# Optimization experiments

Hardware: AMD Instinct MI355X
Metric: run time of the kernel (lower is better)

## Reference

```python
import jax, jax.numpy as jnp
import numpy as np

N_PER_VIEW = 8192
N_VIEWS = 3
N = N_PER_VIEW * N_VIEWS  # 24576 homogeneous nodes
E = 393216
R = 6          # num_relations
B = 8          # num_bases
PROJ = 128     # proj_dim
HEADS = 4
OUT = 32
HO = HEADS * OUT  # 128
LABELS = 4
NEG_SLOPE = 0.2


def setup_inputs() -> dict:
    key = jax.random.key(0)
    ks = jax.random.split(key, 32)
    inp = {}
    inp["x0"] = jax.random.normal(ks[0], (N_PER_VIEW, 2000), jnp.float32)
    inp["x1"] = jax.random.normal(ks[1], (N_PER_VIEW, 1500), jnp.float32)
    inp["x2"] = jax.random.normal(ks[2], (N_PER_VIEW, 500), jnp.float32)
    inp["edge_index"] = jax.random.randint(ks[3], (2, E), 0, N, jnp.int32)
    inp["edge_type"] = jax.random.randint(ks[4], (E,), 0, R, jnp.int32)
    # per-view projection params (pyg.nn.Linear: y = x @ W.T + b)
    inp["Wp0"] = jax.random.normal(ks[5], (PROJ, 2000), jnp.float32) * 0.02
    inp["bp0"] = jnp.zeros((PROJ,), jnp.float32)
    inp["Wp1"] = jax.random.normal(ks[6], (PROJ, 1500), jnp.float32) * 0.02
    inp["bp1"] = jnp.zeros((PROJ,), jnp.float32)
    inp["Wp2"] = jax.random.normal(ks[7], (PROJ, 500), jnp.float32) * 0.02
    inp["bp2"] = jnp.zeros((PROJ,), jnp.float32)
    # RGATConv layer 0 (in = PROJ = 128)
    inp["basis0"] = jax.random.normal(ks[8], (B, PROJ, HO), jnp.float32) * 0.05
    inp["comp0"] = jax.random.normal(ks[9], (R, B), jnp.float32) * 0.3
    inp["q0"] = jax.random.normal(ks[10], (HO, HEADS), jnp.float32) * 0.1
    inp["k0"] = jax.random.normal(ks[11], (HO, HEADS), jnp.float32) * 0.1
    # RGATConv layer 1 (in = HO = 128)
    inp["basis1"] = jax.random.normal(ks[12], (B, HO, HO), jnp.float32) * 0.05
    inp["comp1"] = jax.random.normal(ks[13], (R, B), jnp.float32) * 0.3
    inp["q1"] = jax.random.normal(ks[14], (HO, HEADS), jnp.float32) * 0.1
    inp["k1"] = jax.random.normal(ks[15], (HO, HEADS), jnp.float32) * 0.1
    # LinearIntegration: concat views -> Linear(n_views*HO, n_classes)
    inp["Wc"] = jax.random.normal(ks[16], (LABELS, N_VIEWS * HO), jnp.float32) * 0.05
    inp["bc"] = jnp.zeros((LABELS,), jnp.float32)
    return inp


def _rgat_layer(x, src, dst, edge_type, basis, comp, q, k):
    """PyG RGATConv: basis-decomposed weights, additive self-attention,
    within-relation softmax, mod='f-scaled', heads concatenated."""
    w = jnp.einsum('rb,bio->rio', comp, basis)          # [R, in, H*O]
    xw = jnp.einsum('ni,rio->rno', x, w)                # [R, N, H*O]
    out_j = xw[edge_type, src]                          # [E, H*O] (source msg)
    out_i = xw[edge_type, dst]                          # [E, H*O] (target)
    alpha = jax.nn.leaky_relu(out_i @ q + out_j @ k, NEG_SLOPE)  # [E, H]
    # within-relation softmax over edges sharing (relation, dst)
    seg = edge_type.astype(jnp.int32) * N + dst
    nseg = R * N
    amax = jax.ops.segment_max(alpha, seg, num_segments=nseg)
    ex = jnp.exp(alpha - amax[seg])
    den = jax.ops.segment_sum(ex, seg, num_segments=nseg)
    a = ex / (den[seg] + 1e-16)
    # mod='f-scaled': scale by destination in-degree (over all relations)
    deg = jax.ops.segment_sum(jnp.ones((E,), x.dtype), dst, num_segments=N)
    a = a * deg[dst][:, None]
    msg = (a[:, :, None] * out_j.reshape(E, HEADS, OUT)).reshape(E, HO)
    return jax.ops.segment_sum(msg, dst, num_segments=N)  # [N, H*O]


def _forward(x0, x1, x2, Wp0, bp0, Wp1, bp1, Wp2, bp2,
             basis0, comp0, q0, k0, basis1, comp1, q1, k1, Wc, bc,
             src, dst, edge_type):
    h0 = jax.nn.relu(x0 @ Wp0.T + bp0)
    h1 = jax.nn.relu(x1 @ Wp1.T + bp1)
    h2 = jax.nn.relu(x2 @ Wp2.T + bp2)
    x = jnp.concatenate([h0, h1, h2], axis=0)           # [N, PROJ]
    x = _rgat_layer(x, src, dst, edge_type, basis0, comp0, q0, k0)
    x = _rgat_layer(x, src, dst, edge_type, basis1, comp1, q1, k1)
    views = x.reshape(N_VIEWS, N_PER_VIEW, HO)          # nodes grouped by view
    feat = jnp.transpose(views, (1, 0, 2)).reshape(N_PER_VIEW, N_VIEWS * HO)
    return feat @ Wc.T + bc                              # [N_per_view, LABELS]


def reference(x0, x1, x2, edge_index, edge_type, Wp0, bp0, Wp1, bp1, Wp2, bp2,
              basis0, comp0, q0, k0, basis1, comp1, q1, k1, Wc, bc):
    src, dst = edge_index[0], edge_index[1]
    return _forward(x0, x1, x2, Wp0, bp0, Wp1, bp1, Wp2, bp2,
                    basis0, comp0, q0, k0, basis1, comp1, q1, k1, Wc, bc,
                    src, dst, edge_type)
```

## Files before the change

kernel.cpp:

```cpp
#include <hip/hip_runtime.h>
#include <hip/hip_bf16.h>
#include <math.h>

#define N_NODES 24576
#define NPV 8192
#define E_EDGES 393216
#define R_REL 6
#define B_BASES 8
#define HEADS 4
#define NEG_SLOPE 0.2f
#define NX (N_NODES * 128)
#define NK (N_NODES * R_REL)
#define SCAN_BLOCKS (NK / 256)

typedef unsigned short ushort_t;
using short8 = __attribute__((ext_vector_type(8))) short;
using f32x4 = __attribute__((ext_vector_type(4))) float;

__device__ __forceinline__ float lrelu(float x) { return x >= 0.f ? x : NEG_SLOPE * x; }
__device__ __forceinline__ float b2f(ushort_t u) {
  unsigned int v = ((unsigned int)u) << 16;
  float f;
  __builtin_memcpy(&f, &v, 4);
  return f;
}
__device__ __forceinline__ ushort_t f2b(float f) {
  __hip_bfloat16 h = __float2bfloat16(f);
  ushort_t u;
  __builtin_memcpy(&u, &h, 2);
  return u;
}

__global__ __launch_bounds__(256) void gemm_proj_split(
    const float* __restrict__ x0, const float* __restrict__ x1,
    const float* __restrict__ x2, const float* __restrict__ w0,
    const float* __restrict__ w1, const float* __restrict__ w2,
    float* __restrict__ Ppart) {
  __shared__ __align__(16) ushort_t As[64 * 64];
  __shared__ __align__(16) ushort_t Ws[128 * 64];
  const int z = blockIdx.y;
  const float* A;
  const float* W;
  int K, kstart, ksteps;
  if (z < 4)      { A = x0; W = w0; K = 2000; kstart = z * 512;       ksteps = 8; }
  else if (z < 7) { A = x1; W = w1; K = 1500; kstart = (z - 4) * 512; ksteps = 8; }
  else            { A = x2; W = w2; K = 500;  kstart = (z - 7) * 256; ksteps = 4; }
  const int tid = threadIdx.x;
  const int wave = tid >> 6, lane = tid & 63;
  const int m0 = blockIdx.x * 64;

  f32x4 acc[8];
#pragma unroll
  for (int n = 0; n < 8; ++n) acc[n] = (f32x4){0.f, 0.f, 0.f, 0.f};

  for (int step = 0; step < ksteps; ++step) {
    const int k0 = kstart + (step << 6);
    __syncthreads();
#pragma unroll
    for (int q = 0; q < 2; ++q) {
      int s = q * 256 + tid;
      int row = s >> 3, ch = s & 7;
      int gk = k0 + ((ch ^ (row & 7)) << 3);
      const float* gp = A + (long)(m0 + row) * K + gk;
      short8 o;
      if (gk + 8 <= K) {
        float4 a = *reinterpret_cast<const float4*>(gp);
        float4 b = *reinterpret_cast<const float4*>(gp + 4);
        o[0] = (short)f2b(a.x); o[1] = (short)f2b(a.y);
        o[2] = (short)f2b(a.z); o[3] = (short)f2b(a.w);
        o[4] = (short)f2b(b.x); o[5] = (short)f2b(b.y);
        o[6] = (short)f2b(b.z); o[7] = (short)f2b(b.w);
      } else {
#pragma unroll
        for (int j = 0; j < 8; ++j)
          o[j] = (gk + j < K) ? (short)f2b(gp[j]) : (short)0;
      }
      *reinterpret_cast<short8*>(As + s * 8) = o;
    }
#pragma unroll
    for (int q = 0; q < 4; ++q) {
      int s = q * 256 + tid;
      int row = s >> 3, ch = s & 7;
      int gk = k0 + ((ch ^ (row & 7)) << 3);
      const float* gp = W + (long)row * K + gk;
      short8 o;
      if (gk + 8 <= K) {
        float4 a = *reinterpret_cast<const float4*>(gp);
        float4 b = *reinterpret_cast<const float4*>(gp + 4);
        o[0] = (short)f2b(a.x); o[1] = (short)f2b(a.y);
        o[2] = (short)f2b(a.z); o[3] = (short)f2b(a.w);
        o[4] = (short)f2b(b.x); o[5] = (short)f2b(b.y);
        o[6] = (short)f2b(b.z); o[7] = (short)f2b(b.w);
      } else {
#pragma unroll
        for (int j = 0; j < 8; ++j)
          o[j] = (gk + j < K) ? (short)f2b(gp[j]) : (short)0;
      }
      *reinterpret_cast<short8*>(Ws + s * 8) = o;
    }
    __syncthreads();
#pragma unroll
    for (int kk = 0; kk < 2; ++kk) {
      const int arow = wave * 16 + (lane & 15);
      const int ach = (kk * 4 + (lane >> 4)) ^ (arow & 7);
      short8 afrag = *reinterpret_cast<const short8*>(As + arow * 64 + ach * 8);
#pragma unroll
      for (int n = 0; n < 8; ++n) {
        const int brow = n * 16 + (lane & 15);
        const int bch = (kk * 4 + (lane >> 4)) ^ (brow & 7);
        short8 bfrag = *reinterpret_cast<const short8*>(Ws + brow * 64 + bch * 8);
        acc[n] = __builtin_amdgcn_mfma_f32_16x16x32_bf16(afrag, bfrag, acc[n], 0, 0, 0);
      }
    }
  }
  const int rbase = m0 + wave * 16 + (lane >> 4) * 4;
  const int cb = lane & 15;
  float* out = Ppart + (long)z * NPV * 128;
#pragma unroll
  for (int n = 0; n < 8; ++n) {
    int col = n * 16 + cb;
#pragma unroll
    for (int r = 0; r < 4; ++r)
      out[(long)(rbase + r) * 128 + col] = acc[n][r];
  }
}

__global__ __launch_bounds__(256) void proj_reduce(
    const float* __restrict__ Ppart, const float* __restrict__ b0,
    const float* __restrict__ b1, const float* __restrict__ b2,
    ushort_t* __restrict__ xb) {
  int t = blockIdx.x * blockDim.x + threadIdx.x;
  if (t >= N_NODES * 16) return;
  int n = t >> 4, c0 = (t & 15) * 8;
  int v = n >> 13, m = n & (NPV - 1);
  int zb, zc;
  const float* bias;
  if (v == 0) { zb = 0; zc = 4; bias = b0; }
  else if (v == 1) { zb = 4; zc = 3; bias = b1; }
  else { zb = 7; zc = 2; bias = b2; }
  float s[8];
#pragma unroll
  for (int j = 0; j < 8; ++j) s[j] = bias[c0 + j];
  for (int zz = 0; zz < zc; ++zz) {
    const float* p = Ppart + ((long)(zb + zz) * NPV + m) * 128 + c0;
    float4 a = *reinterpret_cast<const float4*>(p);
    float4 b = *reinterpret_cast<const float4*>(p + 4);
    s[0] += a.x; s[1] += a.y; s[2] += a.z; s[3] += a.w;
    s[4] += b.x; s[5] += b.y; s[6] += b.z; s[7] += b.w;
  }
  short8 o;
#pragma unroll
  for (int j = 0; j < 8; ++j) {
    float vv = s[j] > 0.f ? s[j] : 0.f;
    o[j] = (short)f2b(vv);
  }
  *reinterpret_cast<short8*>(xb + (long)n * 128 + c0) = o;
}

template <bool SPLIT, bool TABLES>
__global__ __launch_bounds__(256) void mfma_gemm_nt(
    const ushort_t* __restrict__ A, const ushort_t* __restrict__ W,
    float* __restrict__ Cacc, ushort_t* __restrict__ Cb,
    int Kp, int kChunk, long strideW, long strideCz,
    const float* __restrict__ qt, const float* __restrict__ kt,
    float* __restrict__ ai, float* __restrict__ aj) {
  __shared__ __align__(16) ushort_t As[64 * 64];
  __shared__ __align__(16) ushort_t Ws[128 * 64];
  const int tid = threadIdx.x;
  const int wave = tid >> 6, lane = tid & 63;
  const int m0 = blockIdx.x * 64;
  const int kbase = blockIdx.y * kChunk;
  const ushort_t* Wz = W + (long)blockIdx.z * strideW;

  f32x4 acc[8];
#pragma unroll
  for (int n = 0; n < 8; ++n) acc[n] = (f32x4){0.f, 0.f, 0.f, 0.f};

  for (int k0 = kbase; k0 < kbase + kChunk; k0 += 64) {
    __syncthreads();
#pragma unroll
    for (int q = 0; q < 2; ++q) {
      int s = q * 256 + tid;
      int row = s >> 3, ch = s & 7;
      int sch = ch ^ (row & 7);
      const ushort_t* g = A + (long)(m0 + row) * Kp + k0 + sch * 8;
      __builtin_amdgcn_global_load_lds(
          (const __attribute__((address_space(1))) unsigned int*)g,
          (__attribute__((address_space(3))) unsigned int*)(As + s * 8), 16, 0, 0);
    }
#pragma unroll
    for (int q = 0; q < 4; ++q) {
      int s = q * 256 + tid;
      int row = s >> 3, ch = s & 7;
      int sch = ch ^ (row & 7);
      const ushort_t* g = Wz + (long)row * Kp + k0 + sch * 8;
      __builtin_amdgcn_global_load_lds(
          (const __attribute__((address_space(1))) unsigned int*)g,
          (__attribute__((address_space(3))) unsigned int*)(Ws + s * 8), 16, 0, 0);
    }
    __syncthreads();
#pragma unroll
    for (int kk = 0; kk < 2; ++kk) {
      const int arow = wave * 16 + (lane & 15);
      const int ach = (kk * 4 + (lane >> 4)) ^ (arow & 7);
      short8 afrag = *reinterpret_cast<const short8*>(As + arow * 64 + ach * 8);
#pragma unroll
      for (int n = 0; n < 8; ++n) {
        const int brow = n * 16 + (lane & 15);
        const int bch = (kk * 4 + (lane >> 4)) ^ (brow & 7);
        short8 bfrag = *reinterpret_cast<const short8*>(Ws + brow * 64 + bch * 8);
        acc[n] = __builtin_amdgcn_mfma_f32_16x16x32_bf16(afrag, bfrag, acc[n], 0, 0, 0);
      }
    }
  }
  const int rbase = m0 + wave * 16 + (lane >> 4) * 4;
  const int cb = lane & 15;
  if (SPLIT) {
#pragma unroll
    for (int n = 0; n < 8; ++n) {
      int col = n * 16 + cb;
#pragma unroll
      for (int r = 0; r < 4; ++r)
        atomicAdd(&Cacc[(long)(rbase + r) * 128 + col], acc[n][r]);
    }
  } else {
    ushort_t* Cz = Cb + (long)blockIdx.z * strideCz;
#pragma unroll
    for (int n = 0; n < 8; ++n) {
      int col = n * 16 + cb;
#pragma unroll
      for (int r = 0; r < 4; ++r)
        Cz[(long)(rbase + r) * 128 + col] = f2b(acc[n][r]);
    }
  }
  if (TABLES) {
    float aq[4][4], ak[4][4];
#pragma unroll
    for (int r = 0; r < 4; ++r)
#pragma unroll
      for (int h = 0; h < 4; ++h) { aq[r][h] = 0.f; ak[r][h] = 0.f; }
#pragma unroll
    for (int n = 0; n < 8; ++n) {
      int col = n * 16 + cb;
      float4 qv = *reinterpret_cast<const float4*>(qt + (long)col * 4);
      float4 kv = *reinterpret_cast<const float4*>(kt + (long)col * 4);
#pragma unroll
      for (int r = 0; r < 4; ++r) {
        float x = acc[n][r];
        aq[r][0] += x * qv.x; aq[r][1] += x * qv.y;
        aq[r][2] += x * qv.z; aq[r][3] += x * qv.w;
        ak[r][0] += x * kv.x; ak[r][1] += x * kv.y;
        ak[r][2] += x * kv.z; ak[r][3] += x * kv.w;
      }
    }
#pragma unroll
    for (int mk = 1; mk < 16; mk <<= 1) {
#pragma unroll
      for (int r = 0; r < 4; ++r)
#pragma unroll
        for (int h = 0; h < 4; ++h) {
          aq[r][h] += __shfl_xor(aq[r][h], mk);
          ak[r][h] += __shfl_xor(ak[r][h], mk);
        }
    }
    int rr = cb >> 2, hh = cb & 3;
    long row = (long)blockIdx.z * N_NODES + rbase + rr;
    ai[row * 4 + hh] = aq[rr][hh];
    aj[row * 4 + hh] = ak[rr][hh];
  }
}

__global__ void fill_f32(float* __restrict__ p, long n, float v) {
  long i = blockIdx.x * (long)blockDim.x + threadIdx.x;
  long stride = (long)gridDim.x * blockDim.x;
  for (; i < n; i += stride) p[i] = v;
}

__global__ void compute_wT_b(const float* __restrict__ comp,
                             const float* __restrict__ basis,
                             ushort_t* __restrict__ wTb) {
  int idx = blockIdx.x * blockDim.x + threadIdx.x;
  if (idx >= R_REL * 128 * 128) return;
  int r = idx >> 14;
  int rem = idx & 16383;
  int o = rem >> 7;
  int i = rem & 127;
  float s = 0.f;
#pragma unroll
  for (int b = 0; b < B_BASES; ++b)
    s += comp[r * B_BASES + b] * basis[((b << 7) + i) * 128 + o];
  wTb[((long)(r << 7) + o) * 128 + i] = f2b(s);
}

__global__ void count_key(const int* __restrict__ dst, const int* __restrict__ et,
                          int* __restrict__ cnt, int E) {
  int e = blockIdx.x * blockDim.x + threadIdx.x;
  if (e < E) atomicAdd(&cnt[dst[e] * R_REL + et[e]], 1);
}

__global__ __launch_bounds__(256) void scan_block(const int* __restrict__ cnt,
                                                  int* __restrict__ start,
                                                  int* __restrict__ blockSums) {
  __shared__ int sm[256];
  const int t = threadIdx.x;
  const int i = blockIdx.x * 256 + t;
  int v = cnt[i];
  sm[t] = v;
  __syncthreads();
  for (int off = 1; off < 256; off <<= 1) {
    int u = (t >= off) ? sm[t - off] : 0;
    __syncthreads();
    sm[t] += u;
    __syncthreads();
  }
  start[i] = sm[t] - v;
  if (t == 255) blockSums[blockIdx.x] = sm[255];
}

__global__ __launch_bounds__(SCAN_BLOCKS) void scan_sums(int* __restrict__ blockSums) {
  __shared__ int sm[SCAN_BLOCKS];
  const int t = threadIdx.x;
  int v = blockSums[t];
  sm[t] = v;
  __syncthreads();
  for (int off = 1; off < SCAN_BLOCKS; off <<= 1) {
    int u = (t >= off) ? sm[t - off] : 0;
    __syncthreads();
    sm[t] += u;
    __syncthreads();
  }
  blockSums[t] = sm[t] - v;
}

__global__ __launch_bounds__(256) void add_offsets(int* __restrict__ start,
                                                   const int* __restrict__ blockSums) {
  int i = blockIdx.x * 256 + threadIdx.x;
  start[i] += blockSums[blockIdx.x];
  if (i == 0) start[NK] = E_EDGES;
}

__global__ void scatter_edges(const int* __restrict__ src, const int* __restrict__ dst,
                              const int* __restrict__ et, const int* __restrict__ start,
                              int* __restrict__ cursor, int* __restrict__ recs, int E) {
  int e = blockIdx.x * blockDim.x + threadIdx.x;
  if (e >= E) return;
  int key = dst[e] * R_REL + et[e];
  int pos = start[key] + atomicAdd(&cursor[key], 1);
  recs[pos] = src[e] | (et[e] << 16);
}

__global__ __launch_bounds__(256) void seg_softmax(
    const int* __restrict__ rstart, const int* __restrict__ recs,
    const float* __restrict__ ai, const float* __restrict__ aj,
    float* __restrict__ coef) {
  int seg = blockIdx.x * blockDim.x + threadIdx.x;
  if (seg >= NK) return;
  int p0 = rstart[seg], p1 = rstart[seg + 1];
  if (p0 == p1) return;
  int d = seg / R_REL, r = seg - d * R_REL;
  float4 av = *reinterpret_cast<const float4*>(ai + ((long)r * N_NODES + d) * 4);
  float degf = (float)(rstart[(d + 1) * R_REL] - rstart[d * R_REL]);
  float m[4] = {-INFINITY, -INFINITY, -INFINITY, -INFINITY};
  float sum[4] = {0.f, 0.f, 0.f, 0.f};
  for (int p = p0; p < p1; ++p) {
    int s = recs[p] & 0xFFFF;
    float4 bv = *reinterpret_cast<const float4*>(aj + ((long)r * N_NODES + s) * 4);
    float al[4] = {lrelu(av.x + bv.x), lrelu(av.y + bv.y),
                   lrelu(av.z + bv.z), lrelu(av.w + bv.w)};
#pragma unroll
    for (int h = 0; h < 4; ++h) {
      float nm = fmaxf(m[h], al[h]);
      sum[h] = sum[h] * __expf(m[h] - nm) + __expf(al[h] - nm);
      m[h] = nm;
    }
  }
  float rs[4];
#pragma unroll
  for (int h = 0; h < 4; ++h) rs[h] = degf / (sum[h] + 1e-16f);
  for (int p = p0; p < p1; ++p) {
    int s = recs[p] & 0xFFFF;
    float4 bv = *reinterpret_cast<const float4*>(aj + ((long)r * N_NODES + s) * 4);
    float al[4] = {lrelu(av.x + bv.x), lrelu(av.y + bv.y),
                   lrelu(av.z + bv.z), lrelu(av.w + bv.w)};
#pragma unroll
    for (int h = 0; h < 4; ++h)
      coef[(long)h * E_EDGES + p] = __expf(al[h] - m[h]) * rs[h];
  }
}

__global__ __launch_bounds__(256) void fused_agg(
    const int* __restrict__ rstart, const int* __restrict__ recs,
    const float* __restrict__ coef, const ushort_t* __restrict__ xwb,
    ushort_t* __restrict__ xb_out, float* __restrict__ fout) {
  const int wave = threadIdx.x >> 6, lane = threadIdx.x & 63;
  const int d = blockIdx.x * 4 + wave;
  const int s0 = rstart[d * R_REL], s1 = rstart[(d + 1) * R_REL];
  const float* cfp = coef + (long)(lane >> 4) * E_EDGES;
  float acc0 = 0.f, acc1 = 0.f;
#pragma unroll 4
  for (int pos = s0; pos < s1; ++pos) {
    int rec = recs[pos];
    float cf = cfp[pos];
    int s = rec & 0xFFFF, r = rec >> 16;
    unsigned int pk = *reinterpret_cast<const unsigned int*>(
        xwb + (((long)r * N_NODES + s) << 7) + 2 * lane);
    acc0 += cf * b2f((ushort_t)(pk & 0xFFFF));
    acc1 += cf * b2f((ushort_t)(pk >> 16));
  }
  if (xb_out) {
    unsigned int po = ((unsigned int)f2b(acc1) << 16) | (unsigned int)f2b(acc0);
    *reinterpret_cast<unsigned int*>(xb_out + ((long)d << 7) + 2 * lane) = po;
  }
  if (fout) {
    *reinterpret_cast<float2*>(fout + ((long)d << 7) + 2 * lane) =
        make_float2(acc0, acc1);
  }
}

__global__ void final_linear(const float* __restrict__ x, const float* __restrict__ Wc,
                             const float* __restrict__ bc, float* __restrict__ out) {
  __shared__ float wcs[4 * 384];
  for (int t = threadIdx.x; t < 4 * 384; t += blockDim.x) wcs[t] = Wc[t];
  __syncthreads();
  int i = blockIdx.x * blockDim.x + threadIdx.x;
  if (i >= NPV) return;
  float acc[4] = {0.f, 0.f, 0.f, 0.f};
  for (int v = 0; v < 3; ++v) {
    const float* xr = x + ((long)v * NPV + i) * 128;
    for (int c = 0; c < 128; c += 4) {
      float4 xv = *reinterpret_cast<const float4*>(xr + c);
#pragma unroll
      for (int l = 0; l < 4; ++l) {
        const float* w = wcs + l * 384 + v * 128 + c;
        acc[l] += xv.x * w[0] + xv.y * w[1] + xv.z * w[2] + xv.w * w[3];
      }
    }
  }
#pragma unroll
  for (int l = 0; l < 4; ++l) out[(long)i * 4 + l] = acc[l] + bc[l];
}

static void run_layer(const ushort_t* xb_in, ushort_t* xb_out, float* fout,
                      const float* basis, const float* comp, const float* q,
                      const float* k, ushort_t* xwb, ushort_t* wTb, float* ai,
                      float* aj, float* coef, const int* rstart, const int* recs,
                      hipStream_t stream) {
  compute_wT_b<<<(R_REL * 128 * 128 + 255) / 256, 256, 0, stream>>>(comp, basis, wTb);
  mfma_gemm_nt<false, true><<<dim3(N_NODES / 64, 1, R_REL), 256, 0, stream>>>(
      xb_in, wTb, nullptr, xwb, 128, 128, 128 * 128, (long)N_NODES * 128,
      q, k, ai, aj);
  seg_softmax<<<(NK + 255) / 256, 256, 0, stream>>>(rstart, recs, ai, aj, coef);
  fused_agg<<<N_NODES / 4, 256, 0, stream>>>(rstart, recs, coef, xwb, xb_out, fout);
}

extern "C" void kernel_launch(void* const* d_in, const int* in_sizes, int n_in,
                              void* d_out, int out_size, void* d_ws, size_t ws_size,
                              hipStream_t stream) {
  const float* x0 = (const float*)d_in[0];
  const float* x1 = (const float*)d_in[1];
  const float* x2 = (const float*)d_in[2];
  const int* edge_index = (const int*)d_in[3];
  const int* edge_type = (const int*)d_in[4];
  const float* Wp0 = (const float*)d_in[5];
  const float* bp0 = (const float*)d_in[6];
  const float* Wp1 = (const float*)d_in[7];
  const float* bp1 = (const float*)d_in[8];
  const float* Wp2 = (const float*)d_in[9];
  const float* bp2 = (const float*)d_in[10];
  const float* basis0 = (const float*)d_in[11];
  const float* comp0 = (const float*)d_in[12];
  const float* q0 = (const float*)d_in[13];
  const float* k0 = (const float*)d_in[14];
  const float* basis1 = (const float*)d_in[15];
  const float* comp1 = (const float*)d_in[16];
  const float* q1 = (const float*)d_in[17];
  const float* k1 = (const float*)d_in[18];
  const float* Wc = (const float*)d_in[19];
  const float* bc = (const float*)d_in[20];

  const int* src = edge_index;
  const int* dst = edge_index + E_EDGES;

  char* w = (char*)d_ws;
  auto alloc = [&](long bytes) {
    char* p = w;
    w += (bytes + 255) & ~255L;
    return p;
  };
  ushort_t* xbA  = (ushort_t*)alloc((long)NX * 2);
  ushort_t* xbB  = (ushort_t*)alloc((long)NX * 2);
  ushort_t* xwb  = (ushort_t*)alloc(9L * NPV * 128 * 4);
  ushort_t* wTb  = (ushort_t*)alloc((long)R_REL * 128 * 128 * 2);
  float* Cacc    = (float*)alloc((long)NX * 4);
  float* ai      = (float*)alloc((long)R_REL * N_NODES * 4 * 4);
  float* aj      = (float*)alloc((long)R_REL * N_NODES * 4 * 4);
  float* coef    = (float*)alloc((long)HEADS * E_EDGES * 4);
  int* cnt       = (int*)alloc((long)NK * 4);
  int* cursor    = (int*)alloc((long)NK * 4);
  int* rstart    = (int*)alloc((long)(NK + 1) * 4);
  int* recs      = (int*)alloc((long)E_EDGES * 4);
  int* blockSums = (int*)alloc((long)SCAN_BLOCKS * 4);
  float* Ppart   = (float*)xwb;

  gemm_proj_split<<<dim3(NPV / 64, 9), 256, 0, stream>>>(
      x0, x1, x2, Wp0, Wp1, Wp2, Ppart);
  proj_reduce<<<(N_NODES * 16 + 255) / 256, 256, 0, stream>>>(
      Ppart, bp0, bp1, bp2, xbA);

  fill_f32<<<96, 256, 0, stream>>>((float*)cnt, 2L * NK, 0.f);
  count_key<<<E_EDGES / 256, 256, 0, stream>>>(dst, edge_type, cnt, E_EDGES);
  scan_block<<<SCAN_BLOCKS, 256, 0, stream>>>(cnt, rstart, blockSums);
  scan_sums<<<1, SCAN_BLOCKS, 0, stream>>>(blockSums);
  add_offsets<<<SCAN_BLOCKS, 256, 0, stream>>>(rstart, blockSums);
  scatter_edges<<<E_EDGES / 256, 256, 0, stream>>>(src, dst, edge_type, rstart,
                                                   cursor, recs, E_EDGES);

  run_layer(xbA, xbB, nullptr, basis0, comp0, q0, k0, xwb, wTb, ai, aj, coef,
            rstart, recs, stream);
  run_layer(xbB, nullptr, Cacc, basis1, comp1, q1, k1, xwb, wTb, ai, aj, coef,
            rstart, recs, stream);

  final_linear<<<(NPV + 255) / 256, 256, 0, stream>>>(Cacc, Wc, bc, (float*)d_out);
}
```

Before: 278.5 us.

## Double-buffer LDS tiles and prefetch next K-slice into registers in projection GEMM

The split-K projection GEMM now loads the next K-slice from global memory into registers while MFMAs run on the current LDS buffer, then converts to bf16 and writes the other LDS buffer. This removes one barrier per step and hides global load latency behind compute. In exchange it doubles shared memory use and adds 48 float registers per thread, which may lower occupancy.

```diff
diff --git a/kernel.cpp b/kernel.cpp
--- a/kernel.cpp
+++ b/kernel.cpp
@@ -36,8 +36,8 @@
     const float* __restrict__ x2, const float* __restrict__ w0,
     const float* __restrict__ w1, const float* __restrict__ w2,
     float* __restrict__ Ppart) {
-  __shared__ __align__(16) ushort_t As[64 * 64];
-  __shared__ __align__(16) ushort_t Ws[128 * 64];
+  __shared__ __align__(16) ushort_t As[2][64 * 64];
+  __shared__ __align__(16) ushort_t Ws[2][128 * 64];
   const int z = blockIdx.y;
   const float* A;
   const float* W;
@@ -53,29 +53,26 @@
 #pragma unroll
   for (int n = 0; n < 8; ++n) acc[n] = (f32x4){0.f, 0.f, 0.f, 0.f};
 
-  for (int step = 0; step < ksteps; ++step) {
-    const int k0 = kstart + (step << 6);
-    __syncthreads();
+  float4 ra[4];
+  float4 rw[8];
+
+  auto LOADR = [&](int k0) {
 #pragma unroll
     for (int q = 0; q < 2; ++q) {
       int s = q * 256 + tid;
       int row = s >> 3, ch = s & 7;
       int gk = k0 + ((ch ^ (row & 7)) << 3);
       const float* gp = A + (long)(m0 + row) * K + gk;
-      short8 o;
       if (gk + 8 <= K) {
-        float4 a = *reinterpret_cast<const float4*>(gp);
-        float4 b = *reinterpret_cast<const float4*>(gp + 4);
-        o[0] = (short)f2b(a.x); o[1] = (short)f2b(a.y);
-        o[2] = (short)f2b(a.z); o[3] = (short)f2b(a.w);
-        o[4] = (short)f2b(b.x); o[5] = (short)f2b(b.y);
-        o[6] = (short)f2b(b.z); o[7] = (short)f2b(b.w);
+        ra[2 * q]     = *reinterpret_cast<const float4*>(gp);
+        ra[2 * q + 1] = *reinterpret_cast<const float4*>(gp + 4);
       } else {
-#pragma unroll
-        for (int j = 0; j < 8; ++j)
-          o[j] = (gk + j < K) ? (short)f2b(gp[j]) : (short)0;
+        float t[8];
+#pragma unroll
+        for (int j = 0; j < 8; ++j) t[j] = (gk + j < K) ? gp[j] : 0.f;
+        ra[2 * q]     = make_float4(t[0], t[1], t[2], t[3]);
+        ra[2 * q + 1] = make_float4(t[4], t[5], t[6], t[7]);
       }
-      *reinterpret_cast<short8*>(As + s * 8) = o;
     }
 #pragma unroll
     for (int q = 0; q < 4; ++q) {
@@ -83,36 +80,73 @@
       int row = s >> 3, ch = s & 7;
       int gk = k0 + ((ch ^ (row & 7)) << 3);
       const float* gp = W + (long)row * K + gk;
+      if (gk + 8 <= K) {
+        rw[2 * q]     = *reinterpret_cast<const float4*>(gp);
+        rw[2 * q + 1] = *reinterpret_cast<const float4*>(gp + 4);
+      } else {
+        float t[8];
+#pragma unroll
+        for (int j = 0; j < 8; ++j) t[j] = (gk + j < K) ? gp[j] : 0.f;
+        rw[2 * q]     = make_float4(t[0], t[1], t[2], t[3]);
+        rw[2 * q + 1] = make_float4(t[4], t[5], t[6], t[7]);
+      }
+    }
+  };
+
+  auto WRITELDS = [&](int buf) {
+#pragma unroll
+    for (int q = 0; q < 2; ++q) {
+      int s = q * 256 + tid;
       short8 o;
-      if (gk + 8 <= K) {
-        float4 a = *reinterpret_cast<const float4*>(gp);
-        float4 b = *reinterpret_cast<const float4*>(gp + 4);
-        o[0] = (short)f2b(a.x); o[1] = (short)f2b(a.y);
-        o[2] = (short)f2b(a.z); o[3] = (short)f2b(a.w);
-        o[4] = (short)f2b(b.x); o[5] = (short)f2b(b.y);
-        o[6] = (short)f2b(b.z); o[7] = (short)f2b(b.w);
-      } else {
-#pragma unroll
-        for (int j = 0; j < 8; ++j)
-          o[j] = (gk + j < K) ? (short)f2b(gp[j]) : (short)0;
-      }
-      *reinterpret_cast<short8*>(Ws + s * 8) = o;
-    }
-    __syncthreads();
+      o[0] = (short)f2b(ra[2 * q].x); o[1] = (short)f2b(ra[2 * q].y);
+      o[2] = (short)f2b(ra[2 * q].z); o[3] = (short)f2b(ra[2 * q].w);
+      o[4] = (short)f2b(ra[2 * q + 1].x); o[5] = (short)f2b(ra[2 * q + 1].y);
+      o[6] = (short)f2b(ra[2 * q + 1].z); o[7] = (short)f2b(ra[2 * q + 1].w);
+      *reinterpret_cast<short8*>(As[buf] + s * 8) = o;
+    }
+#pragma unroll
+    for (int q = 0; q < 4; ++q) {
+      int s = q * 256 + tid;
+      short8 o;
+      o[0] = (short)f2b(rw[2 * q].x); o[1] = (short)f2b(rw[2 * q].y);
+      o[2] = (short)f2b(rw[2 * q].z); o[3] = (short)f2b(rw[2 * q].w);
+      o[4] = (short)f2b(rw[2 * q + 1].x); o[5] = (short)f2b(rw[2 * q + 1].y);
+      o[6] = (short)f2b(rw[2 * q + 1].z); o[7] = (short)f2b(rw[2 * q + 1].w);
+      *reinterpret_cast<short8*>(Ws[buf] + s * 8) = o;
+    }
+  };
+
+  auto MFMA = [&](int buf) {
 #pragma unroll
     for (int kk = 0; kk < 2; ++kk) {
       const int arow = wave * 16 + (lane & 15);
       const int ach = (kk * 4 + (lane >> 4)) ^ (arow & 7);
-      short8 afrag = *reinterpret_cast<const short8*>(As + arow * 64 + ach * 8);
+      short8 afrag = *reinterpret_cast<const short8*>(As[buf] + arow * 64 + ach * 8);
 #pragma unroll
       for (int n = 0; n < 8; ++n) {
         const int brow = n * 16 + (lane & 15);
         const int bch = (kk * 4 + (lane >> 4)) ^ (brow & 7);
-        short8 bfrag = *reinterpret_cast<const short8*>(Ws + brow * 64 + bch * 8);
+        short8 bfrag = *reinterpret_cast<const short8*>(Ws[buf] + brow * 64 + bch * 8);
         acc[n] = __builtin_amdgcn_mfma_f32_16x16x32_bf16(afrag, bfrag, acc[n], 0, 0, 0);
       }
     }
-  }
+  };
+
+  LOADR(kstart);
+  WRITELDS(0);
+  __syncthreads();
+  int cur = 0;
+  for (int step = 0; step < ksteps; ++step) {
+    bool more = (step + 1 < ksteps);
+    if (more) LOADR(kstart + ((step + 1) << 6));
+    MFMA(cur);
+    if (more) {
+      WRITELDS(cur ^ 1);
+      __syncthreads();
+    }
+    cur ^= 1;
+  }
+
   const int rbase = m0 + wave * 16 + (lane >> 4) * 4;
   const int cb = lane & 15;
   float* out = Ppart + (long)z * NPV * 128;
```

After: 278.0 us. About the same (-0.2%).

## Pre-convert projection weights to padded bf16 and stream tiles via direct-to-LDS loads

Applied to the files above, without the earlier changes.

Projection weights are converted once per call into a zero-padded bf16 buffer, so the GEMM can fetch weight tiles with direct global-to-LDS loads and skip per-block conversion. Activation tiles are also loaded as fp32 straight into LDS, using an XOR swizzle over 16 chunks, and converted to bf16 when the fragments are read. This cuts register staging and repeated conversion in the load path. In exchange it adds three small conversion launches, doubles the A-tile LDS footprint, and handles tail K chunks through a slower scalar path.

```diff
diff --git a/kernel.cpp b/kernel.cpp
--- a/kernel.cpp
+++ b/kernel.cpp
@@ -12,6 +12,7 @@
 #define NX (N_NODES * 128)
 #define NK (N_NODES * R_REL)
 #define SCAN_BLOCKS (NK / 256)
+#define WPAD 2048
 
 typedef unsigned short ushort_t;
 using short8 = __attribute__((ext_vector_type(8))) short;
@@ -31,20 +32,57 @@
   return u;
 }
 
+__global__ void cvt_pad_bf16(const float* __restrict__ in, ushort_t* __restrict__ out,
+                             int M, int K, int Kp) {
+  int kp8 = Kp >> 3;
+  int total = M * kp8;
+  for (int t = blockIdx.x * blockDim.x + threadIdx.x; t < total;
+       t += gridDim.x * blockDim.x) {
+    int row = t / kp8;
+    int c0 = (t - row * kp8) * 8;
+    short8 o;
+    if (c0 + 7 < K) {
+      const float4 a = *reinterpret_cast<const float4*>(in + (long)row * K + c0);
+      const float4 b = *reinterpret_cast<const float4*>(in + (long)row * K + c0 + 4);
+      o[0] = (short)f2b(a.x); o[1] = (short)f2b(a.y);
+      o[2] = (short)f2b(a.z); o[3] = (short)f2b(a.w);
+      o[4] = (short)f2b(b.x); o[5] = (short)f2b(b.y);
+      o[6] = (short)f2b(b.z); o[7] = (short)f2b(b.w);
+    } else {
+#pragma unroll
+      for (int j = 0; j < 8; ++j) {
+        int c = c0 + j;
+        float v = (c < K) ? in[(long)row * K + c] : 0.f;
+        o[j] = (short)f2b(v);
+      }
+    }
+    *reinterpret_cast<short8*>(out + (long)row * Kp + c0) = o;
+  }
+}
+
 __global__ __launch_bounds__(256) void gemm_proj_split(
     const float* __restrict__ x0, const float* __restrict__ x1,
-    const float* __restrict__ x2, const float* __restrict__ w0,
-    const float* __restrict__ w1, const float* __restrict__ w2,
+    const float* __restrict__ x2, const ushort_t* __restrict__ wb,
     float* __restrict__ Ppart) {
-  __shared__ __align__(16) ushort_t As[64 * 64];
+  __shared__ __align__(16) float Af[64 * 64];
   __shared__ __align__(16) ushort_t Ws[128 * 64];
   const int z = blockIdx.y;
   const float* A;
-  const float* W;
-  int K, kstart, ksteps;
-  if (z < 4)      { A = x0; W = w0; K = 2000; kstart = z * 512;       ksteps = 8; }
-  else if (z < 7) { A = x1; W = w1; K = 1500; kstart = (z - 4) * 512; ksteps = 8; }
-  else            { A = x2; W = w2; K = 500;  kstart = (z - 7) * 256; ksteps = 4; }
+  const ushort_t* W;
+  int K, kstart, kend;
+  if (z < 4) {
+    A = x0; W = wb; K = 2000; kstart = z * 512;
+  } else if (z < 7) {
+    A = x1; W = wb + 128L * WPAD; K = 1500; kstart = (z - 4) * 512;
+  } else {
+    A = x2; W = wb + 256L * WPAD; K = 500; kstart = (z - 7) * 256;
+  }
+  kend = kstart + ((z < 7) ? 512 : 256);
+  if (kend > K) kend = K;
+  const int nfull = (kend - kstart) >> 6;
+  const int tail = (kend - kstart) & 63;
+  const int nsteps = nfull + (tail ? 1 : 0);
+
   const int tid = threadIdx.x;
   const int wave = tid >> 6, lane = tid & 63;
   const int m0 = blockIdx.x * 64;
@@ -53,57 +91,59 @@
 #pragma unroll
   for (int n = 0; n < 8; ++n) acc[n] = (f32x4){0.f, 0.f, 0.f, 0.f};
 
-  for (int step = 0; step < ksteps; ++step) {
+  for (int step = 0; step < nsteps; ++step) {
     const int k0 = kstart + (step << 6);
     __syncthreads();
-#pragma unroll
-    for (int q = 0; q < 2; ++q) {
-      int s = q * 256 + tid;
-      int row = s >> 3, ch = s & 7;
-      int gk = k0 + ((ch ^ (row & 7)) << 3);
-      const float* gp = A + (long)(m0 + row) * K + gk;
-      short8 o;
-      if (gk + 8 <= K) {
-        float4 a = *reinterpret_cast<const float4*>(gp);
-        float4 b = *reinterpret_cast<const float4*>(gp + 4);
-        o[0] = (short)f2b(a.x); o[1] = (short)f2b(a.y);
-        o[2] = (short)f2b(a.z); o[3] = (short)f2b(a.w);
-        o[4] = (short)f2b(b.x); o[5] = (short)f2b(b.y);
-        o[6] = (short)f2b(b.z); o[7] = (short)f2b(b.w);
-      } else {
-#pragma unroll
-        for (int j = 0; j < 8; ++j)
-          o[j] = (gk + j < K) ? (short)f2b(gp[j]) : (short)0;
-      }
-      *reinterpret_cast<short8*>(As + s * 8) = o;
+    if (step < nfull) {
+#pragma unroll
+      for (int q = 0; q < 4; ++q) {
+        int s = q * 256 + tid;
+        int row = s >> 4, ch = s & 15;
+        int sch = ch ^ (row & 15);
+        const float* g = A + (long)(m0 + row) * K + k0 + sch * 4;
+        __builtin_amdgcn_global_load_lds(
+            (const __attribute__((address_space(1))) unsigned int*)g,
+            (__attribute__((address_space(3))) unsigned int*)(Af + s * 4), 16, 0, 0);
+      }
+    } else {
+#pragma unroll
+      for (int q = 0; q < 4; ++q) {
+        int s = q * 256 + tid;
+        int row = s >> 4, ch = s & 15;
+        int sch = ch ^ (row & 15);
+        int gk = k0 + sch * 4;
+        const float* gp = A + (long)(m0 + row) * K + gk;
+        float4 v = make_float4(0.f, 0.f, 0.f, 0.f);
+#pragma unroll
+        for (int j = 0; j < 4; ++j)
+          if (gk + j < kend) (&v.x)[j] = gp[j];
+        *reinterpret_cast<float4*>(Af + s * 4) = v;
+      }
     }
 #pragma unroll
     for (int q = 0; q < 4; ++q) {
       int s = q * 256 + tid;
       int row = s >> 3, ch = s & 7;
-      int gk = k0 + ((ch ^ (row & 7)) << 3);
-      const float* gp = W + (long)row * K + gk;
-      short8 o;
-      if (gk + 8 <= K) {
-        float4 a = *reinterpret_cast<const float4*>(gp);
-        float4 b = *reinterpret_cast<const float4*>(gp + 4);
-        o[0] = (short)f2b(a.x); o[1] = (short)f2b(a.y);
-        o[2] = (short)f2b(a.z); o[3] = (short)f2b(a.w);
-        o[4] = (short)f2b(b.x); o[5] = (short)f2b(b.y);
-        o[6] = (short)f2b(b.z); o[7] = (short)f2b(b.w);
-      } else {
-#pragma unroll
-        for (int j = 0; j < 8; ++j)
-          o[j] = (gk + j < K) ? (short)f2b(gp[j]) : (short)0;
-      }
-      *reinterpret_cast<short8*>(Ws + s * 8) = o;
+      int sch = ch ^ (row & 7);
+      const ushort_t* g = W + (long)row * WPAD + k0 + sch * 8;
+      __builtin_amdgcn_global_load_lds(
+          (const __attribute__((address_space(1))) unsigned int*)g,
+          (__attribute__((address_space(3))) unsigned int*)(Ws + s * 8), 16, 0, 0);
     }
     __syncthreads();
 #pragma unroll
     for (int kk = 0; kk < 2; ++kk) {
       const int arow = wave * 16 + (lane & 15);
-      const int ach = (kk * 4 + (lane >> 4)) ^ (arow & 7);
-      short8 afrag = *reinterpret_cast<const short8*>(As + arow * 64 + ach * 8);
+      const int t = kk * 4 + (lane >> 4);
+      const int sc0 = (2 * t) ^ (arow & 15);
+      const int sc1 = (2 * t + 1) ^ (arow & 15);
+      f32x4 a0 = *reinterpret_cast<const f32x4*>(Af + arow * 64 + sc0 * 4);
+      f32x4 a1 = *reinterpret_cast<const f32x4*>(Af + arow * 64 + sc1 * 4);
+      short8 afrag;
+      afrag[0] = (short)f2b(a0[0]); afrag[1] = (short)f2b(a0[1]);
+      afrag[2] = (short)f2b(a0[2]); afrag[3] = (short)f2b(a0[3]);
+      afrag[4] = (short)f2b(a1[0]); afrag[5] = (short)f2b(a1[1]);
+      afrag[6] = (short)f2b(a1[2]); afrag[7] = (short)f2b(a1[3]);
 #pragma unroll
       for (int n = 0; n < 8; ++n) {
         const int brow = n * 16 + (lane & 15);
@@ -491,6 +531,7 @@
   ushort_t* xbB  = (ushort_t*)alloc((long)NX * 2);
   ushort_t* xwb  = (ushort_t*)alloc(9L * NPV * 128 * 4);
   ushort_t* wTb  = (ushort_t*)alloc((long)R_REL * 128 * 128 * 2);
+  ushort_t* padW = (ushort_t*)alloc(3L * 128 * WPAD * 2);
   float* Cacc    = (float*)alloc((long)NX * 4);
   float* ai      = (float*)alloc((long)R_REL * N_NODES * 4 * 4);
   float* aj      = (float*)alloc((long)R_REL * N_NODES * 4 * 4);
@@ -502,8 +543,12 @@
   int* blockSums = (int*)alloc((long)SCAN_BLOCKS * 4);
   float* Ppart   = (float*)xwb;
 
+  cvt_pad_bf16<<<128, 256, 0, stream>>>(Wp0, padW + 0L * 128 * WPAD, 128, 2000, WPAD);
+  cvt_pad_bf16<<<128, 256, 0, stream>>>(Wp1, padW + 1L * 128 * WPAD, 128, 1500, WPAD);
+  cvt_pad_bf16<<<128, 256, 0, stream>>>(Wp2, padW + 2L * 128 * WPAD, 128, 500, WPAD);
+
   gemm_proj_split<<<dim3(NPV / 64, 9), 256, 0, stream>>>(
-      x0, x1, x2, Wp0, Wp1, Wp2, Ppart);
+      x0, x1, x2, padW, Ppart);
   proj_reduce<<<(N_NODES * 16 + 255) / 256, 256, 0, stream>>>(
       Ppart, bp0, bp1, bp2, xbA);
 
```

Measured after the change: 278.8 us. No clear change (+0.1%).
